# Optimization experiments

Measured on AMD Instinct MI355X. Metric: run time of the kernel, lower is better.

## Reference

```python
import jax, jax.numpy as jnp
import numpy as np

N_NODES = 50000
N_EDGES = 800000
N_GRAPHS = 512
H = 64
F_NODE = 32
F_EDGE = 8
N_CLASSES = 10
EPS = 1e-5


def _bn(x, w, b):
    # BatchNorm1d in training mode: batch stats, biased variance
    m = jnp.mean(x, axis=0)
    v = jnp.mean(jnp.square(x - m), axis=0)
    return (x - m) * jax.lax.rsqrt(v + EPS) * w + b


def setup_inputs() -> dict:
    key = jax.random.key(0)
    ks = jax.random.split(key, 12)
    s = 0.02
    inp = {
        "x": jax.random.normal(ks[0], (N_NODES, F_NODE), jnp.float32),
        "edge_attr": jax.random.normal(ks[1], (N_EDGES, F_EDGE), jnp.float32),
        "edge_index": jax.random.randint(ks[2], (2, N_EDGES), 0, N_NODES),
        "batch": jnp.sort(jax.random.randint(ks[3], (N_NODES,), 0, N_GRAPHS)),
        "bn_feat_w": jnp.ones((F_NODE,), jnp.float32),
        "bn_feat_b": jnp.full((F_NODE,), 1e-4, jnp.float32),
        "Wn0": jax.random.normal(ks[4], (F_NODE, H), jnp.float32) * s,
        "bn0": jnp.zeros((H,), jnp.float32),
        "We0": jax.random.normal(ks[5], (2 * H + F_EDGE, H), jnp.float32) * s,
        "be0": jnp.zeros((H,), jnp.float32),
        "bns_w": jnp.ones((3, H), jnp.float32),
        "bns_b": jnp.full((3, H), 1e-4, jnp.float32),
        "Wn": jax.random.normal(ks[6], (3, H, H), jnp.float32) * s,
        "Wnb": jnp.zeros((3, H), jnp.float32),
        "We": jax.random.normal(ks[7], (3, 3 * H, H), jnp.float32) * s,
        "Web": jnp.zeros((3, H), jnp.float32),
        "bn_fc_w": jnp.ones((H,), jnp.float32),
        "bn_fc_b": jnp.full((H,), 1e-4, jnp.float32),
        "Wfc": jax.random.normal(ks[8], (H, H), jnp.float32) * s,
        "bfc": jnp.zeros((H,), jnp.float32),
        "bn_hid_w": jnp.ones((H,), jnp.float32),
        "bn_hid_b": jnp.full((H,), 1e-4, jnp.float32),
        "Wcls": jax.random.normal(ks[9], (H, N_CLASSES), jnp.float32) * s,
        "bcls": jnp.zeros((N_CLASSES,), jnp.float32),
    }
    return inp


def reference(x, edge_attr, edge_index, batch, bn_feat_w, bn_feat_b, Wn0, bn0,
              We0, be0, bns_w, bns_b, Wn, Wnb, We, Web, bn_fc_w, bn_fc_b,
              Wfc, bfc, bn_hid_w, bn_hid_b, Wcls, bcls):
    src, dst = edge_index[0], edge_index[1]
    n = x.shape[0]
    # symmetric GCN edge normalization (edge_norm=True)
    deg = jax.ops.segment_sum(jnp.ones_like(src, jnp.float32), dst, num_segments=n)
    dinv = jax.lax.rsqrt(jnp.maximum(deg, 1.0))
    norm = (dinv[src] * dinv[dst])[:, None]  # [E,1]

    # feature conv (gfn=True: linear transforms only, no propagation)
    h = _bn(x, bn_feat_w, bn_feat_b) @ Wn0 + bn0  # [N,H]
    e = (h[src] @ We0[:H] + h[dst] @ We0[H:2 * H]
         + edge_attr @ We0[2 * H:] + be0)         # [E,H]
    h = jax.nn.relu(h)
    e = jax.nn.relu(e)

    # stacked edge-gated GCN convs: BN -> conv(gather/scatter) -> ReLU
    for i in range(3):
        ht = _bn(h, bns_w[i], bns_b[i]) @ Wn[i] + Wnb[i]          # [N,H]
        hs = ht[src]                                               # [E,H] gather
        ei = (hs @ We[i, :H] + ht[dst] @ We[i, H:2 * H]
              + e @ We[i, 2 * H:] + Web[i])                        # [E,H]
        msg = norm * hs * jax.nn.sigmoid(ei)                       # edge-gated message
        h = jax.nn.relu(jax.ops.segment_sum(msg, dst, num_segments=n))

    # global_add_pool over graphs
    g = jax.ops.segment_sum(h, batch, num_segments=N_GRAPHS)       # [G,H]
    g = jax.nn.relu(_bn(g, bn_fc_w, bn_fc_b) @ Wfc + bfc)
    g = _bn(g, bn_hid_w, bn_hid_b) @ Wcls + bcls
    return jax.nn.log_softmax(g, axis=-1)
```

## Files before the change

kernel.cpp:

```cpp
#include <hip/hip_runtime.h>
#include <hip/hip_bf16.h>

#define N_NODESC 50000
#define N_EDGESC 800000
#define N_GRAPHSC 512
#define HDIM 64
#define FNODE 32
#define FEDGE 8
#define NCLS 10
#define BN_EPS 1e-5f
#define SCAN_B 256
#define SCAN_G 196
#define NPW 8

typedef __bf16 bf16x8 __attribute__((ext_vector_type(8)));
typedef float f32x4 __attribute__((ext_vector_type(4)));
typedef unsigned int uint32;

static __device__ __forceinline__ float bcast(float v, int k) {
  return __uint_as_float(__builtin_amdgcn_readlane(__float_as_uint(v), k));
}
static __device__ __forceinline__ unsigned short f2bu(float f) {
  __hip_bfloat16 b = __float2bfloat16(f);
  return *reinterpret_cast<unsigned short*>(&b);
}
static __device__ __forceinline__ float bu2f(unsigned short u) {
  __hip_bfloat16 b;
  *reinterpret_cast<unsigned short*>(&b) = u;
  return __bfloat162float(b);
}

__global__ void k_deg(const int* __restrict__ dst, uint32* __restrict__ degi) {
  int e = blockIdx.x * blockDim.x + threadIdx.x;
  if (e < N_EDGESC) atomicAdd(&degi[dst[e]], 1u);
}

__global__ void k_dinv(const uint32* __restrict__ degi, float* __restrict__ dinv) {
  int n = blockIdx.x * blockDim.x + threadIdx.x;
  if (n < N_NODESC) dinv[n] = rsqrtf(fmaxf((float)degi[n], 1.0f));
}

__global__ void k_scan1(const uint32* __restrict__ degi, uint32* __restrict__ ptr,
                        uint32* __restrict__ bsum) {
  __shared__ uint32 s[SCAN_B];
  int t = threadIdx.x;
  int i = blockIdx.x * SCAN_B + t;
  uint32 v = (i < N_NODESC) ? degi[i] : 0u;
  s[t] = v; __syncthreads();
  for (int off = 1; off < SCAN_B; off <<= 1) {
    uint32 x = (t >= off) ? s[t - off] : 0u; __syncthreads();
    s[t] += x; __syncthreads();
  }
  if (i < N_NODESC) ptr[i] = s[t] - v;
  if (t == SCAN_B - 1) bsum[blockIdx.x] = s[t];
}

__global__ void k_scan2(uint32* __restrict__ bsum) {
  __shared__ uint32 s[256];
  int t = threadIdx.x;
  uint32 v = (t < SCAN_G) ? bsum[t] : 0u;
  s[t] = v; __syncthreads();
  for (int off = 1; off < 256; off <<= 1) {
    uint32 x = (t >= off) ? s[t - off] : 0u; __syncthreads();
    s[t] += x; __syncthreads();
  }
  if (t < SCAN_G) bsum[t] = s[t] - v;
}

__global__ void k_scan3(uint32* __restrict__ ptr, const uint32* __restrict__ bsum) {
  int i = blockIdx.x * SCAN_B + threadIdx.x;
  if (i < N_NODESC) ptr[i] += bsum[blockIdx.x];
  if (blockIdx.x == 0 && threadIdx.x == 0) ptr[N_NODESC] = N_EDGESC;
}

__global__ void k_scatter(const int* __restrict__ src, const int* __restrict__ dst,
                          const float* __restrict__ ea, const float* __restrict__ dinv,
                          const uint32* __restrict__ ptr, uint32* __restrict__ cursor,
                          int* __restrict__ srcs, int* __restrict__ dsts,
                          float* __restrict__ ea_s, float* __restrict__ normf) {
  int e = blockIdx.x * blockDim.x + threadIdx.x;
  if (e < N_EDGESC) {
    int d = dst[e];
    int s = src[e];
    float4 a0 = *reinterpret_cast<const float4*>(ea + (size_t)e * FEDGE);
    float4 a1 = *reinterpret_cast<const float4*>(ea + (size_t)e * FEDGE + 4);
    uint32 r = atomicAdd(&cursor[d], 1u);
    uint32 i = ptr[d] + r;
    srcs[i] = s;
    dsts[i] = d;
    normf[i] = dinv[s] * dinv[d];
    *reinterpret_cast<float4*>(ea_s + (size_t)i * FEDGE) = a0;
    *reinterpret_cast<float4*>(ea_s + (size_t)i * FEDGE + 4) = a1;
  }
}

template <int C>
__global__ void k_colstats(const float* __restrict__ in, int nrows, float* __restrict__ stats) {
  const int RPB = 256 / C;
  int tid = threadIdx.x;
  int col = tid % C;
  int rowOff = tid / C;
  float s = 0.f, s2 = 0.f;
  for (int r = blockIdx.x * RPB + rowOff; r < nrows; r += gridDim.x * RPB) {
    float v = in[r * C + col];
    s += v; s2 += v * v;
  }
  __shared__ float ls[256], ls2[256];
  ls[tid] = s; ls2[tid] = s2;
  __syncthreads();
  for (int off = 128; off >= C; off >>= 1) {
    if (tid < off) { ls[tid] += ls[tid + off]; ls2[tid] += ls2[tid + off]; }
    __syncthreads();
  }
  if (tid < C) {
    atomicAdd(&stats[tid], ls[tid]);
    atomicAdd(&stats[C + tid], ls2[tid]);
  }
}

template <int CIN, int COUT>
__global__ void k_foldbn(const float* __restrict__ stats, float invN,
                         const float* __restrict__ bnw, const float* __restrict__ bnb,
                         const float* __restrict__ W, const float* __restrict__ bias,
                         float* __restrict__ Wf, float* __restrict__ bf) {
  __shared__ float a[CIN], sh[CIN];
  int tid = threadIdx.x;
  if (tid < CIN) {
    float m = stats[tid] * invN;
    float v = stats[CIN + tid] * invN - m * m;
    float inv = rsqrtf(v + BN_EPS);
    float aa = bnw[tid] * inv;
    a[tid] = aa;
    sh[tid] = bnb[tid] - m * aa;
  }
  __syncthreads();
  for (int i = tid; i < CIN * COUT; i += 256) {
    int r = i / COUT;
    Wf[i] = a[r] * W[i];
  }
  if (tid < COUT) {
    float acc = bias ? bias[tid] : 0.f;
    for (int r = 0; r < CIN; ++r) acc += sh[r] * W[r * COUT + tid];
    bf[tid] = acc;
  }
}

template <int K, bool RELU>
__global__ void k_nodemm(const float* __restrict__ in, int nrows,
                         const float* __restrict__ W, const float* __restrict__ bias,
                         float* __restrict__ out) {
  int tid = threadIdx.x;
  int lane = tid & 63;
  float w[K];
#pragma unroll
  for (int k = 0; k < K; ++k) w[k] = W[k * 64 + lane];
  float bv = bias ? bias[lane] : 0.f;
  int wave = (blockIdx.x * blockDim.x + tid) >> 6;
  int nwaves = (gridDim.x * blockDim.x) >> 6;
  for (int r = wave; r < nrows; r += nwaves) {
    float rv = (lane < K) ? in[(size_t)r * K + lane] : 0.f;
    float acc = bv;
#pragma unroll
    for (int k = 0; k < K; ++k) acc = fmaf(bcast(rv, k), w[k], acc);
    if (RELU) acc = fmaxf(acc, 0.f);
    out[(size_t)r * 64 + lane] = acc;
  }
}

__global__ void __launch_bounds__(256, 2) k_stage0(
    const float* __restrict__ x, int nrows,
    const float* __restrict__ Wf, const float* __restrict__ bfv,
    const float* __restrict__ WA, const float* __restrict__ bA,
    const float* __restrict__ WB,
    float* __restrict__ h, unsigned short* __restrict__ hAb,
    unsigned short* __restrict__ hBb) {
  int tid = threadIdx.x;
  int lane = tid & 63;
  float w0[FNODE], wA[64], wB[64];
#pragma unroll
  for (int k = 0; k < FNODE; ++k) w0[k] = Wf[k * 64 + lane];
#pragma unroll
  for (int k = 0; k < 64; ++k) wA[k] = WA[k * 64 + lane];
#pragma unroll
  for (int k = 0; k < 64; ++k) wB[k] = WB[k * 64 + lane];
  float b0 = bfv[lane];
  float b2 = bA[lane];
  int wave = (blockIdx.x * blockDim.x + tid) >> 6;
  int nwaves = (gridDim.x * blockDim.x) >> 6;
  for (int r = wave; r < nrows; r += nwaves) {
    float xv = (lane < FNODE) ? x[(size_t)r * FNODE + lane] : 0.f;
    float t0 = b0;
#pragma unroll
    for (int k = 0; k < FNODE; ++k) t0 = fmaf(bcast(xv, k), w0[k], t0);
    float aA = b2, aB = 0.f;
#pragma unroll
    for (int k = 0; k < 64; ++k) {
      float tb = bcast(t0, k);
      aA = fmaf(tb, wA[k], aA);
      aB = fmaf(tb, wB[k], aB);
    }
    h[(size_t)r * 64 + lane] = fmaxf(t0, 0.f);
    hAb[(size_t)r * 64 + lane] = f2bu(aA);
    hBb[(size_t)r * 64 + lane] = f2bu(aB);
  }
}

__global__ void __launch_bounds__(256, 2) k_node3(
    const float* __restrict__ h, int nrows,
    const float* __restrict__ stats, float invN,
    const float* __restrict__ bnw, const float* __restrict__ bnb,
    const float* __restrict__ Wn_i, const float* __restrict__ Wnb_i,
    const float* __restrict__ WA, const float* __restrict__ Wab,
    const float* __restrict__ WB,
    uint32* __restrict__ htP, unsigned short* __restrict__ htBb) {
  __shared__ float a_s[64], sh_s[64];
  int tid = threadIdx.x;
  int lane = tid & 63;
  if (tid < 64) {
    float m = stats[tid] * invN;
    float v = stats[64 + tid] * invN - m * m;
    float inv = rsqrtf(v + BN_EPS);
    float aa = bnw[tid] * inv;
    a_s[tid] = aa;
    sh_s[tid] = bnb[tid] - m * aa;
  }
  __syncthreads();
  float w1[64], w2[64], w3[64];
  float b1 = Wnb_i[lane];
#pragma unroll
  for (int k = 0; k < 64; ++k) {
    float raw = Wn_i[k * 64 + lane];
    w1[k] = a_s[k] * raw;
    b1 = fmaf(sh_s[k], raw, b1);
  }
#pragma unroll
  for (int k = 0; k < 64; ++k) w2[k] = WA[k * 64 + lane];
#pragma unroll
  for (int k = 0; k < 64; ++k) w3[k] = WB[k * 64 + lane];
  float b2 = Wab[lane];
  int cperm = (lane & 15) * 4 + (lane >> 4);
  int wave = (blockIdx.x * blockDim.x + tid) >> 6;
  int nwaves = (gridDim.x * blockDim.x) >> 6;
  for (int r = wave; r < nrows; r += nwaves) {
    float hv = h[(size_t)r * 64 + lane];
    float t1 = b1;
#pragma unroll
    for (int k = 0; k < 64; ++k) t1 = fmaf(bcast(hv, k), w1[k], t1);
    float t2 = b2;
    float t3 = 0.f;
#pragma unroll
    for (int k = 0; k < 64; ++k) {
      float tb = bcast(t1, k);
      t2 = fmaf(tb, w2[k], t2);
      t3 = fmaf(tb, w3[k], t3);
    }
    htP[(size_t)r * 64 + cperm] = ((uint32)f2bu(t2) << 16) | (uint32)f2bu(t1);
    htBb[(size_t)r * 64 + lane] = f2bu(t3);
  }
}

__global__ void k_edgeinit(const unsigned short* __restrict__ hAb,
                           const unsigned short* __restrict__ hBb,
                           const float* __restrict__ ea_s, const float* __restrict__ Wc,
                           const int* __restrict__ srcs, const int* __restrict__ dsts,
                           __hip_bfloat16* __restrict__ ebf) {
  int tid = threadIdx.x;
  int lane = tid & 63;
  float w[FEDGE];
#pragma unroll
  for (int k = 0; k < FEDGE; ++k) w[k] = Wc[k * 64 + lane];
  int wave = (blockIdx.x * blockDim.x + tid) >> 6;
  int nwaves = (gridDim.x * blockDim.x) >> 6;
  const int nquads = N_EDGESC / 4;
  int per = (nquads + nwaves - 1) / nwaves;
  int p0 = wave * per;
  int p1 = min(p0 + per, nquads);
  for (int pr = p0; pr < p1; ++pr) {
    int e = 4 * pr;
    int s0 = srcs[e],     d0 = dsts[e];
    int s1 = srcs[e + 1], d1 = dsts[e + 1];
    int s2 = srcs[e + 2], d2 = dsts[e + 2];
    int s3 = srcs[e + 3], d3 = dsts[e + 3];
    bool el = (lane < FEDGE);
    float av0 = el ? ea_s[(size_t)e * FEDGE + lane] : 0.f;
    float av1 = el ? ea_s[(size_t)(e + 1) * FEDGE + lane] : 0.f;
    float av2 = el ? ea_s[(size_t)(e + 2) * FEDGE + lane] : 0.f;
    float av3 = el ? ea_s[(size_t)(e + 3) * FEDGE + lane] : 0.f;
    unsigned short a0 = hAb[s0 * 64 + lane], b0 = hBb[d0 * 64 + lane];
    unsigned short a1 = hAb[s1 * 64 + lane], b1 = hBb[d1 * 64 + lane];
    unsigned short a2 = hAb[s2 * 64 + lane], b2 = hBb[d2 * 64 + lane];
    unsigned short a3 = hAb[s3 * 64 + lane], b3 = hBb[d3 * 64 + lane];
    float acc0 = bu2f(a0) + bu2f(b0);
    float acc1 = bu2f(a1) + bu2f(b1);
    float acc2 = bu2f(a2) + bu2f(b2);
    float acc3 = bu2f(a3) + bu2f(b3);
#pragma unroll
    for (int k = 0; k < FEDGE; ++k) {
      acc0 = fmaf(bcast(av0, k), w[k], acc0);
      acc1 = fmaf(bcast(av1, k), w[k], acc1);
      acc2 = fmaf(bcast(av2, k), w[k], acc2);
      acc3 = fmaf(bcast(av3, k), w[k], acc3);
    }
    unsigned short* ob = reinterpret_cast<unsigned short*>(ebf);
    __builtin_nontemporal_store(f2bu(fmaxf(acc0, 0.f)), ob + (size_t)e * 64 + lane);
    __builtin_nontemporal_store(f2bu(fmaxf(acc1, 0.f)), ob + (size_t)(e + 1) * 64 + lane);
    __builtin_nontemporal_store(f2bu(fmaxf(acc2, 0.f)), ob + (size_t)(e + 2) * 64 + lane);
    __builtin_nontemporal_store(f2bu(fmaxf(acc3, 0.f)), ob + (size_t)(e + 3) * 64 + lane);
  }
}

__global__ void __launch_bounds__(256, 4) k_conv_mfma(
    const __hip_bfloat16* __restrict__ ebf,
    const float* __restrict__ We2,
    const uint32* __restrict__ htP, const unsigned short* __restrict__ htBb,
    const float* __restrict__ normf,
    const int* __restrict__ srcs, const int* __restrict__ dsts,
    const uint32* __restrict__ ptr,
    float* __restrict__ hout) {
  __shared__ float lds_acc[4][NPW * 65];
  __shared__ float lds_htB[4][NPW * 65];
  const int tid = threadIdx.x;
  const int lane = tid & 63;
  const int w = tid >> 6;
  const int m = lane & 15;
  const int kg = lane >> 4;

  int wave = blockIdx.x * 4 + w;
  int n0 = wave * NPW;
  if (n0 >= N_NODESC) return;

  bf16x8 b[4][2];
#pragma unroll
  for (int t = 0; t < 4; ++t)
#pragma unroll
    for (int s = 0; s < 2; ++s)
#pragma unroll
      for (int j = 0; j < 8; ++j) {
        int k = s * 32 + kg * 8 + j;
        int c = t * 16 + m;
        b[t][s][j] = (__bf16)We2[k * 64 + c];
      }

  float* acc_l = lds_acc[w];
  float* htB_l = lds_htB[w];
#pragma unroll
  for (int r = 0; r < NPW; ++r) {
    acc_l[r * 65 + lane] = 0.f;
    htB_l[r * 65 + lane] = bu2f(htBb[(size_t)(n0 + r) * 64 + lane]);
  }

  int e0 = (int)ptr[n0];
  int eend = (int)ptr[n0 + NPW];
  int tb0 = e0 & ~15;

  float run[4] = {0.f, 0.f, 0.f, 0.f};
  int dcur = -1, rcur = 0;

  int rb = tb0 + kg * 4;
  int4 sev = *reinterpret_cast<const int4*>(srcs + rb);
  int4 dev = *reinterpret_cast<const int4*>(dsts + rb);
  float4 nev = *reinterpret_cast<const float4*>(normf + rb);

  for (int tb = tb0; tb < eend; tb += 16) {
    int4 sev_n = sev, dev_n = dev;
    float4 nev_n = nev;
    int tbn = tb + 16;
    if (tbn < eend) {
      int rbn = tbn + kg * 4;
      sev_n = *reinterpret_cast<const int4*>(srcs + rbn);
      dev_n = *reinterpret_cast<const int4*>(dsts + rbn);
      nev_n = *reinterpret_cast<const float4*>(normf + rbn);
    }
    const bf16x8* arow = reinterpret_cast<const bf16x8*>(ebf + (size_t)(tb + m) * 64 + kg * 8);
    bf16x8 a0 = __builtin_nontemporal_load(arow);
    bf16x8 a1 = __builtin_nontemporal_load(arow + 4);
    int se[4] = {sev.x, sev.y, sev.z, sev.w};
    int de[4] = {dev.x, dev.y, dev.z, dev.w};
    float ne[4] = {nev.x, nev.y, nev.z, nev.w};
    uint4 pv[4];
#pragma unroll
    for (int j = 0; j < 4; ++j)
      pv[j] = *reinterpret_cast<const uint4*>(htP + (size_t)se[j] * 64 + m * 4);

    f32x4 acc[4];
#pragma unroll
    for (int t = 0; t < 4; ++t) {
      f32x4 z = {0.f, 0.f, 0.f, 0.f};
      acc[t] = __builtin_amdgcn_mfma_f32_16x16x32_bf16(a0, b[t][0], z, 0, 0, 0);
      acc[t] = __builtin_amdgcn_mfma_f32_16x16x32_bf16(a1, b[t][1], acc[t], 0, 0, 0);
    }

    int rbj = tb + kg * 4;
#pragma unroll
    for (int j = 0; j < 4; ++j) {
      int eidx = rbj + j;
      bool valid = (eidx >= e0) && (eidx < eend);
      if (valid) {
        if (de[j] != dcur) {
          if (dcur >= 0) {
#pragma unroll
            for (int t = 0; t < 4; ++t) {
              atomicAdd(&acc_l[rcur * 65 + t * 16 + m], run[t]);
              run[t] = 0.f;
            }
          }
          dcur = de[j];
          rcur = dcur - n0;
        }
        uint32 pd[4] = {pv[j].x, pv[j].y, pv[j].z, pv[j].w};
#pragma unroll
        for (int t = 0; t < 4; ++t) {
          int c = t * 16 + m;
          float gate = acc[t][j] + bu2f((unsigned short)(pd[t] >> 16)) + htB_l[rcur * 65 + c];
          float sig = 1.0f / (1.0f + __expf(-gate));
          run[t] = fmaf(ne[j] * bu2f((unsigned short)(pd[t] & 0xffffu)), sig, run[t]);
        }
      }
    }
    sev = sev_n; dev = dev_n; nev = nev_n;
  }
  if (dcur >= 0) {
#pragma unroll
    for (int t = 0; t < 4; ++t)
      atomicAdd(&acc_l[rcur * 65 + t * 16 + m], run[t]);
  }
#pragma unroll
  for (int r = 0; r < NPW; ++r)
    hout[(size_t)(n0 + r) * 64 + lane] = fmaxf(acc_l[r * 65 + lane], 0.f);
}

__global__ void k_pool(const float* __restrict__ h, const int* __restrict__ batch,
                       float* __restrict__ g) {
  int lane = threadIdx.x & 63;
  int wave = (blockIdx.x * blockDim.x + threadIdx.x) >> 6;
  int nwaves = (gridDim.x * blockDim.x) >> 6;
  int chunk = (N_NODESC + nwaves - 1) / nwaves;
  int r0 = wave * chunk;
  int r1 = min(r0 + chunk, N_NODESC);
  if (r0 >= r1) return;
  int cur = batch[r0];
  float acc = 0.f;
  for (int r = r0; r < r1; ++r) {
    int b = batch[r];
    if (b != cur) {
      atomicAdd(&g[cur * 64 + lane], acc);
      acc = 0.f;
      cur = b;
    }
    acc += h[r * 64 + lane];
  }
  atomicAdd(&g[cur * 64 + lane], acc);
}

__global__ void k_cls(const float* __restrict__ g2, const float* __restrict__ Wc,
                      const float* __restrict__ bc, float* __restrict__ out) {
  int r = blockIdx.x * blockDim.x + threadIdx.x;
  if (r >= N_GRAPHSC) return;
  float z[NCLS];
#pragma unroll
  for (int c = 0; c < NCLS; ++c) z[c] = bc[c];
  for (int k = 0; k < HDIM; ++k) {
    float v = g2[r * HDIM + k];
#pragma unroll
    for (int c = 0; c < NCLS; ++c) z[c] = fmaf(v, Wc[k * NCLS + c], z[c]);
  }
  float m = z[0];
#pragma unroll
  for (int c = 1; c < NCLS; ++c) m = fmaxf(m, z[c]);
  float ssum = 0.f;
#pragma unroll
  for (int c = 0; c < NCLS; ++c) ssum += __expf(z[c] - m);
  float l = __logf(ssum);
#pragma unroll
  for (int c = 0; c < NCLS; ++c) out[r * NCLS + c] = z[c] - m - l;
}

extern "C" void kernel_launch(void* const* d_in, const int* in_sizes, int n_in,
                              void* d_out, int out_size, void* d_ws, size_t ws_size,
                              hipStream_t stream) {
  const float* x         = (const float*)d_in[0];
  const float* edge_attr = (const float*)d_in[1];
  const int*   ei        = (const int*)d_in[2];
  const int*   batch     = (const int*)d_in[3];
  const float* bn_feat_w = (const float*)d_in[4];
  const float* bn_feat_b = (const float*)d_in[5];
  const float* Wn0       = (const float*)d_in[6];
  const float* bn0       = (const float*)d_in[7];
  const float* We0       = (const float*)d_in[8];
  const float* be0       = (const float*)d_in[9];
  const float* bns_w     = (const float*)d_in[10];
  const float* bns_b     = (const float*)d_in[11];
  const float* Wn        = (const float*)d_in[12];
  const float* Wnb       = (const float*)d_in[13];
  const float* We        = (const float*)d_in[14];
  const float* Web       = (const float*)d_in[15];
  const float* bn_fc_w   = (const float*)d_in[16];
  const float* bn_fc_b   = (const float*)d_in[17];
  const float* Wfc       = (const float*)d_in[18];
  const float* bfc       = (const float*)d_in[19];
  const float* bn_hid_w  = (const float*)d_in[20];
  const float* bn_hid_b  = (const float*)d_in[21];
  const float* Wcls      = (const float*)d_in[22];
  const float* bcls      = (const float*)d_in[23];
  float* out = (float*)d_out;
  const int* src = ei;
  const int* dst = ei + N_EDGESC;

  char* p = (char*)d_ws;
  auto carve = [&](size_t bytes) {
    char* q = p;
    p += (bytes + 255) & ~(size_t)255;
    return q;
  };
  __hip_bfloat16* ebf = (__hip_bfloat16*)carve((size_t)N_EDGESC * 64 * 2);
  float* h    = (float*)carve((size_t)N_NODESC * 64 * 4);
  uint32* htP = (uint32*)carve((size_t)N_NODESC * 64 * 4);
  unsigned short* htBb = (unsigned short*)carve((size_t)N_NODESC * 64 * 2);
  unsigned short* hAb  = (unsigned short*)carve((size_t)N_NODESC * 64 * 2);
  unsigned short* hBb  = (unsigned short*)carve((size_t)N_NODESC * 64 * 2);
  float* dinv = (float*)carve((size_t)N_NODESC * 4);
  float* g    = (float*)carve((size_t)N_GRAPHSC * 64 * 4);
  float* g2   = (float*)carve((size_t)N_GRAPHSC * 64 * 4);
  float* stats= (float*)carve(6 * 128 * 4);
  float* Wf   = (float*)carve(64 * 64 * 4);
  float* bf   = (float*)carve(64 * 4);
  uint32* degi   = (uint32*)carve((size_t)50176 * 4);
  uint32* ptr    = (uint32*)carve((size_t)50176 * 4);
  uint32* cursor = (uint32*)carve((size_t)50176 * 4);
  uint32* bsum   = (uint32*)carve(256 * 4);
  int* srcs  = (int*)carve((size_t)N_EDGESC * 4);
  int* dsts  = (int*)carve((size_t)N_EDGESC * 4);
  float* ea_s  = (float*)carve((size_t)N_EDGESC * FEDGE * 4);
  float* normf = (float*)carve((size_t)N_EDGESC * 4);

  float* st_x  = stats;
  float* st_h0 = stats + 128;
  float* st_h1 = stats + 256;
  float* st_h2 = stats + 384;
  float* st_g  = stats + 512;
  float* st_g2 = stats + 640;

  hipMemsetAsync(degi, 0, (size_t)3 * 50176 * 4, stream);
  hipMemsetAsync(stats, 0, 6 * 128 * 4, stream);

  k_deg<<<(N_EDGESC + 255) / 256, 256, 0, stream>>>(dst, degi);
  k_dinv<<<(N_NODESC + 255) / 256, 256, 0, stream>>>(degi, dinv);
  k_scan1<<<SCAN_G, SCAN_B, 0, stream>>>(degi, ptr, bsum);
  k_scan2<<<1, 256, 0, stream>>>(bsum);
  k_scan3<<<SCAN_G, SCAN_B, 0, stream>>>(ptr, bsum);
  k_scatter<<<(N_EDGESC + 255) / 256, 256, 0, stream>>>(src, dst, edge_attr, dinv, ptr, cursor,
                                                        srcs, dsts, ea_s, normf);

  k_colstats<FNODE><<<256, 256, 0, stream>>>(x, N_NODESC, st_x);
  k_foldbn<FNODE, HDIM><<<1, 256, 0, stream>>>(st_x, 1.f / N_NODESC, bn_feat_w, bn_feat_b, Wn0, bn0, Wf, bf);
  k_stage0<<<512, 256, 0, stream>>>(x, N_NODESC, Wf, bf, We0, be0, We0 + 64 * 64, h, hAb, hBb);
  k_edgeinit<<<1024, 256, 0, stream>>>(hAb, hBb, ea_s, We0 + 128 * 64, srcs, dsts, ebf);
  k_colstats<HDIM><<<256, 256, 0, stream>>>(h, N_NODESC, st_h0);

  const int convBlocks = (N_NODESC / NPW + 3) / 4;
  float* slots[3] = {st_h0, st_h1, st_h2};
  for (int i = 0; i < 3; ++i) {
    const float* WeI = We + (size_t)i * 192 * 64;
    k_node3<<<512, 256, 0, stream>>>(h, N_NODESC, slots[i], 1.f / N_NODESC,
                                     bns_w + i * 64, bns_b + i * 64,
                                     Wn + (size_t)i * 64 * 64, Wnb + i * 64,
                                     WeI, Web + i * 64, WeI + 64 * 64, htP, htBb);
    k_conv_mfma<<<convBlocks, 256, 0, stream>>>(ebf, WeI + 128 * 64, htP, htBb, normf,
                                                srcs, dsts, ptr, h);
    if (i < 2) k_colstats<HDIM><<<256, 256, 0, stream>>>(h, N_NODESC, slots[i + 1]);
  }

  hipMemsetAsync(g, 0, N_GRAPHSC * 64 * 4, stream);
  k_pool<<<64, 256, 0, stream>>>(h, batch, g);
  k_colstats<HDIM><<<32, 256, 0, stream>>>(g, N_GRAPHSC, st_g);
  k_foldbn<HDIM, HDIM><<<1, 256, 0, stream>>>(st_g, 1.f / N_GRAPHSC, bn_fc_w, bn_fc_b, Wfc, bfc, Wf, bf);
  k_nodemm<HDIM, true><<<128, 256, 0, stream>>>(g, N_GRAPHSC, Wf, bf, g2);
  k_colstats<HDIM><<<32, 256, 0, stream>>>(g2, N_GRAPHSC, st_g2);
  k_foldbn<HDIM, NCLS><<<1, 256, 0, stream>>>(st_g2, 1.f / N_GRAPHSC, bn_hid_w, bn_hid_b, Wcls, bcls, Wf, bf);
  k_cls<<<(N_GRAPHSC + 255) / 256, 256, 0, stream>>>(g2, Wf, bf, out);
}
```

Measured before the change: 793.2 us.

## Fuse BN column stats into conv epilogue, halve nodes per wave, reshape prefetch

The conv kernel now accumulates per-column sum and sum-of-squares of its ReLU output in LDS and atomically adds them to the global stats buffer. This removes the two separate colstats launches and their rereads of h. Nodes per wave drop from 8 to 4, which doubles the number of waves for better load balance. The srcs/dsts/norm prefetch in the conv loop is removed in favour of direct loads, and the edge-init kernel now prefetches the next quad's indices. The risks are more global atomics and a changed latency-hiding profile; 50000/16 divides exactly, so the bounds check can be dropped.

```diff
diff --git a/kernel.cpp b/kernel.cpp
--- a/kernel.cpp
+++ b/kernel.cpp
@@ -11,7 +11,7 @@
 #define BN_EPS 1e-5f
 #define SCAN_B 256
 #define SCAN_G 196
-#define NPW 8
+#define NPW 4
 
 typedef __bf16 bf16x8 __attribute__((ext_vector_type(8)));
 typedef float f32x4 __attribute__((ext_vector_type(4)));
@@ -275,21 +275,26 @@
   int per = (nquads + nwaves - 1) / nwaves;
   int p0 = wave * per;
   int p1 = min(p0 + per, nquads);
+  if (p0 >= p1) return;
+  bool el = (lane < FEDGE);
+  int e = 4 * p0;
+  int s0 = srcs[e], s1 = srcs[e + 1], s2 = srcs[e + 2], s3 = srcs[e + 3];
+  int d0 = dsts[e], d1 = dsts[e + 1], d2 = dsts[e + 2], d3 = dsts[e + 3];
   for (int pr = p0; pr < p1; ++pr) {
-    int e = 4 * pr;
-    int s0 = srcs[e],     d0 = dsts[e];
-    int s1 = srcs[e + 1], d1 = dsts[e + 1];
-    int s2 = srcs[e + 2], d2 = dsts[e + 2];
-    int s3 = srcs[e + 3], d3 = dsts[e + 3];
-    bool el = (lane < FEDGE);
+    e = 4 * pr;
+    unsigned short a0 = hAb[s0 * 64 + lane], b0 = hBb[d0 * 64 + lane];
+    unsigned short a1 = hAb[s1 * 64 + lane], b1 = hBb[d1 * 64 + lane];
+    unsigned short a2 = hAb[s2 * 64 + lane], b2 = hBb[d2 * 64 + lane];
+    unsigned short a3 = hAb[s3 * 64 + lane], b3 = hBb[d3 * 64 + lane];
     float av0 = el ? ea_s[(size_t)e * FEDGE + lane] : 0.f;
     float av1 = el ? ea_s[(size_t)(e + 1) * FEDGE + lane] : 0.f;
     float av2 = el ? ea_s[(size_t)(e + 2) * FEDGE + lane] : 0.f;
     float av3 = el ? ea_s[(size_t)(e + 3) * FEDGE + lane] : 0.f;
-    unsigned short a0 = hAb[s0 * 64 + lane], b0 = hBb[d0 * 64 + lane];
-    unsigned short a1 = hAb[s1 * 64 + lane], b1 = hBb[d1 * 64 + lane];
-    unsigned short a2 = hAb[s2 * 64 + lane], b2 = hBb[d2 * 64 + lane];
-    unsigned short a3 = hAb[s3 * 64 + lane], b3 = hBb[d3 * 64 + lane];
+    if (pr + 1 < p1) {
+      int en = 4 * (pr + 1);
+      s0 = srcs[en]; s1 = srcs[en + 1]; s2 = srcs[en + 2]; s3 = srcs[en + 3];
+      d0 = dsts[en]; d1 = dsts[en + 1]; d2 = dsts[en + 2]; d3 = dsts[en + 3];
+    }
     float acc0 = bu2f(a0) + bu2f(b0);
     float acc1 = bu2f(a1) + bu2f(b1);
     float acc2 = bu2f(a2) + bu2f(b2);
@@ -316,9 +321,10 @@
     const float* __restrict__ normf,
     const int* __restrict__ srcs, const int* __restrict__ dsts,
     const uint32* __restrict__ ptr,
-    float* __restrict__ hout) {
+    float* __restrict__ hout, float* __restrict__ stats) {
   __shared__ float lds_acc[4][NPW * 65];
   __shared__ float lds_htB[4][NPW * 65];
+  __shared__ float st_s[64], st_s2[64];
   const int tid = threadIdx.x;
   const int lane = tid & 63;
   const int w = tid >> 6;
@@ -327,7 +333,9 @@
 
   int wave = blockIdx.x * 4 + w;
   int n0 = wave * NPW;
-  if (n0 >= N_NODESC) return;
+
+  if (stats && tid < 64) { st_s[tid] = 0.f; st_s2[tid] = 0.f; }
+  if (stats) __syncthreads();
 
   bf16x8 b[4][2];
 #pragma unroll
@@ -356,24 +364,14 @@
   float run[4] = {0.f, 0.f, 0.f, 0.f};
   int dcur = -1, rcur = 0;
 
-  int rb = tb0 + kg * 4;
-  int4 sev = *reinterpret_cast<const int4*>(srcs + rb);
-  int4 dev = *reinterpret_cast<const int4*>(dsts + rb);
-  float4 nev = *reinterpret_cast<const float4*>(normf + rb);
-
   for (int tb = tb0; tb < eend; tb += 16) {
-    int4 sev_n = sev, dev_n = dev;
-    float4 nev_n = nev;
-    int tbn = tb + 16;
-    if (tbn < eend) {
-      int rbn = tbn + kg * 4;
-      sev_n = *reinterpret_cast<const int4*>(srcs + rbn);
-      dev_n = *reinterpret_cast<const int4*>(dsts + rbn);
-      nev_n = *reinterpret_cast<const float4*>(normf + rbn);
-    }
     const bf16x8* arow = reinterpret_cast<const bf16x8*>(ebf + (size_t)(tb + m) * 64 + kg * 8);
     bf16x8 a0 = __builtin_nontemporal_load(arow);
     bf16x8 a1 = __builtin_nontemporal_load(arow + 4);
+    int rb = tb + kg * 4;
+    int4 sev = *reinterpret_cast<const int4*>(srcs + rb);
+    int4 dev = *reinterpret_cast<const int4*>(dsts + rb);
+    float4 nev = *reinterpret_cast<const float4*>(normf + rb);
     int se[4] = {sev.x, sev.y, sev.z, sev.w};
     int de[4] = {dev.x, dev.y, dev.z, dev.w};
     float ne[4] = {nev.x, nev.y, nev.z, nev.w};
@@ -390,10 +388,9 @@
       acc[t] = __builtin_amdgcn_mfma_f32_16x16x32_bf16(a1, b[t][1], acc[t], 0, 0, 0);
     }
 
-    int rbj = tb + kg * 4;
 #pragma unroll
     for (int j = 0; j < 4; ++j) {
-      int eidx = rbj + j;
+      int eidx = rb + j;
       bool valid = (eidx >= e0) && (eidx < eend);
       if (valid) {
         if (de[j] != dcur) {
@@ -417,16 +414,26 @@
         }
       }
     }
-    sev = sev_n; dev = dev_n; nev = nev_n;
   }
   if (dcur >= 0) {
 #pragma unroll
     for (int t = 0; t < 4; ++t)
       atomicAdd(&acc_l[rcur * 65 + t * 16 + m], run[t]);
   }
-#pragma unroll
-  for (int r = 0; r < NPW; ++r)
-    hout[(size_t)(n0 + r) * 64 + lane] = fmaxf(acc_l[r * 65 + lane], 0.f);
+  float s = 0.f, s2 = 0.f;
+#pragma unroll
+  for (int r = 0; r < NPW; ++r) {
+    float v = fmaxf(acc_l[r * 65 + lane], 0.f);
+    hout[(size_t)(n0 + r) * 64 + lane] = v;
+    s += v; s2 += v * v;
+  }
+  if (stats) {
+    atomicAdd(&st_s[lane], s);
+    atomicAdd(&st_s2[lane], s2);
+    __syncthreads();
+    if (tid < 64) atomicAdd(&stats[tid], st_s[tid]);
+    else if (tid < 128) atomicAdd(&stats[tid], st_s2[tid - 64]);
+  }
 }
 
 __global__ void k_pool(const float* __restrict__ h, const int* __restrict__ batch,
@@ -557,17 +564,17 @@
   k_edgeinit<<<1024, 256, 0, stream>>>(hAb, hBb, ea_s, We0 + 128 * 64, srcs, dsts, ebf);
   k_colstats<HDIM><<<256, 256, 0, stream>>>(h, N_NODESC, st_h0);
 
-  const int convBlocks = (N_NODESC / NPW + 3) / 4;
-  float* slots[3] = {st_h0, st_h1, st_h2};
+  const int convBlocks = N_NODESC / (NPW * 4);
+  float* inSlot[3]  = {st_h0, st_h1, st_h2};
+  float* outSlot[3] = {st_h1, st_h2, nullptr};
   for (int i = 0; i < 3; ++i) {
     const float* WeI = We + (size_t)i * 192 * 64;
-    k_node3<<<512, 256, 0, stream>>>(h, N_NODESC, slots[i], 1.f / N_NODESC,
+    k_node3<<<512, 256, 0, stream>>>(h, N_NODESC, inSlot[i], 1.f / N_NODESC,
                                      bns_w + i * 64, bns_b + i * 64,
                                      Wn + (size_t)i * 64 * 64, Wnb + i * 64,
                                      WeI, Web + i * 64, WeI + 64 * 64, htP, htBb);
     k_conv_mfma<<<convBlocks, 256, 0, stream>>>(ebf, WeI + 128 * 64, htP, htBb, normf,
-                                                srcs, dsts, ptr, h);
-    if (i < 2) k_colstats<HDIM><<<256, 256, 0, stream>>>(h, N_NODESC, slots[i + 1]);
+                                                srcs, dsts, ptr, h, outSlot[i]);
   }
 
   hipMemsetAsync(g, 0, N_GRAPHSC * 64 * 4, stream);
```

After: 782.7 us. About the same (-1.3%).
